# Kernel optimization log

Hardware: AMD Instinct MI355X
Metric: run time of the kernel (lower is better)

Reference implementation:

```python
import jax, jax.numpy as jnp
import numpy as np

B, S, H, F, E, K = 2, 2048, 1024, 2816, 8, 2

def setup_inputs() -> dict:
    key = jax.random.key(0)
    k0, k1, k2, k3, k4 = jax.random.split(key, 5)
    return {
        "hidden_states": jax.random.normal(k0, (B, S, H), dtype=jnp.float32),
        "router_w": jax.random.normal(k1, (E, H), dtype=jnp.float32) * (1.0 / np.sqrt(H)),
        "w_gate": jax.random.normal(k2, (E, H, F), dtype=jnp.float32) * (1.0 / np.sqrt(H)),
        "w_up": jax.random.normal(k3, (E, H, F), dtype=jnp.float32) * (1.0 / np.sqrt(H)),
        "w_down": jax.random.normal(k4, (E, F, H), dtype=jnp.float32) * (1.0 / np.sqrt(F)),
    }

def reference(hidden_states, router_w, w_gate, w_up, w_down):
    # Router: logits [B,S,E], top-k routing with softmax over the k selected logits.
    router_logits = jnp.einsum("bsh,eh->bse", hidden_states, router_w)
    topk_values, topk_indices = jax.lax.top_k(router_logits, K)  # [B,S,K]
    topk_weights = jax.nn.softmax(topk_values.astype(jnp.float32), axis=-1).astype(hidden_states.dtype)

    x = hidden_states.reshape(-1, H)            # [T,H], T = B*S
    flat_idx = topk_indices.reshape(-1, K)      # [T,K] (int)
    flat_w = topk_weights.reshape(-1, K)        # [T,K]

    mixed = jnp.zeros_like(x)
    for e in range(E):  # small fixed expert loop; tokens fully vectorized
        # per-token combine weight for expert e (0 if not routed here)
        w_e = jnp.sum(jnp.where(flat_idx == e, flat_w, jnp.zeros_like(flat_w)), axis=-1)[:, None]
        # SwiGLU expert MLP: down(silu(gate(x)) * up(x))
        y = (jax.nn.silu(x @ w_gate[e]) * (x @ w_up[e])) @ w_down[e]
        mixed = mixed + w_e * y
    mixed_output = mixed.reshape(hidden_states.shape)

    # Load-balancing aux loss (Switch-style)
    router_probs = jax.nn.softmax(router_logits.astype(jnp.float32), axis=-1)
    P = router_probs.mean(axis=(0, 1))                                   # [E]
    f = jax.nn.one_hot(topk_indices, E, dtype=jnp.float32).mean(axis=(0, 1, 2))  # [E]
    aux_loss = E * jnp.sum(f * P)
    return mixed_output, aux_loss
```

## Files before the change

### kernel.cpp

```cpp
#include <hip/hip_runtime.h>
#include <hip/hip_bf16.h>
#include <stdint.h>

#define T_TOK 4096
#define H_DIM 1024
#define F_DIM 2816
#define E_NUM 8
#define ROWS_CAP 9216
#define TOTAL_MT 72

typedef float  f32x4  __attribute__((ext_vector_type(4)));
typedef __bf16 bf16x8 __attribute__((ext_vector_type(8)));

__device__ __forceinline__ unsigned short f32_bf16(float f) {
  union { float f; unsigned u; } v; v.f = f;
  unsigned r = v.u + 0x7fffu + ((v.u >> 16) & 1u);
  return (unsigned short)(r >> 16);
}

__device__ __forceinline__ void async16(const void* g, void* l) {
  __builtin_amdgcn_global_load_lds(
      (__attribute__((address_space(1))) void*)(g),
      (__attribute__((address_space(3))) void*)(l),
      16, 0, 0);
}

__device__ __forceinline__ f32x4 mfma16(bf16x8 a, bf16x8 b, f32x4 c) {
  return __builtin_amdgcn_mfma_f32_16x16x32_bf16(a, b, c, 0, 0, 0);
}


__global__ __launch_bounds__(256) void conv_x_kernel(const float* __restrict__ x,
                                                     unsigned short* __restrict__ xb) {
  int i = blockIdx.x * 256 + threadIdx.x;
  float4 v = ((const float4*)x)[i];
  ushort4 o;
  o.x = f32_bf16(v.x); o.y = f32_bf16(v.y); o.z = f32_bf16(v.z); o.w = f32_bf16(v.w);
  ((ushort4*)xb)[i] = o;
}

__global__ __launch_bounds__(256) void transpose_conv(const float* __restrict__ src,
                                                      unsigned short* __restrict__ dst,
                                                      int R, int C) {
  __shared__ float tile[32][33];
  int e = blockIdx.z;
  const float* s = src + (size_t)e * R * C;
  unsigned short* d = dst + (size_t)e * R * C;
  int r0 = blockIdx.y * 32, c0 = blockIdx.x * 32;
  int tx = threadIdx.x, ty = threadIdx.y;
#pragma unroll
  for (int k = 0; k < 4; k++)
    tile[ty + 8 * k][tx] = s[(size_t)(r0 + ty + 8 * k) * C + (c0 + tx)];
  __syncthreads();
#pragma unroll
  for (int k = 0; k < 4; k++)
    d[(size_t)(c0 + ty + 8 * k) * R + (r0 + tx)] = f32_bf16(tile[tx][ty + 8 * k]);
}


__global__ __launch_bounds__(256) void router_kernel(const float* __restrict__ x,
                                                     const float* __restrict__ rw,
                                                     int* __restrict__ t2i,
                                                     float* __restrict__ t2w,
                                                     int* __restrict__ counts,
                                                     float* __restrict__ psum) {
  __shared__ float srw[E_NUM * H_DIM];
  __shared__ float sP[E_NUM];
  __shared__ int sC[E_NUM];
  int tid = threadIdx.x;
  for (int i = tid; i < E_NUM * H_DIM; i += 256) srw[i] = rw[i];
  if (tid < E_NUM) { sP[tid] = 0.f; sC[tid] = 0; }
  __syncthreads();
  int w = tid >> 6, lane = tid & 63;
  for (int it = 0; it < 16; ++it) {
    int t = blockIdx.x * 64 + w * 16 + it;
    float acc[E_NUM];
#pragma unroll
    for (int e = 0; e < E_NUM; e++) acc[e] = 0.f;
    const float* xr = x + (size_t)t * H_DIM;
    for (int h = lane; h < H_DIM; h += 64) {
      float xv = xr[h];
#pragma unroll
      for (int e = 0; e < E_NUM; e++) acc[e] += xv * srw[e * H_DIM + h];
    }
#pragma unroll
    for (int e = 0; e < E_NUM; e++) {
      float v = acc[e];
      for (int o = 32; o > 0; o >>= 1) v += __shfl_down(v, o, 64);
      acc[e] = __shfl(v, 0, 64);
    }
    if (lane == 0) {
      float mx = acc[0];
#pragma unroll
      for (int e = 1; e < E_NUM; e++) mx = fmaxf(mx, acc[e]);
      float pr[E_NUM], s = 0.f;
#pragma unroll
      for (int e = 0; e < E_NUM; e++) { pr[e] = __expf(acc[e] - mx); s += pr[e]; }
      float inv = 1.f / s;
#pragma unroll
      for (int e = 0; e < E_NUM; e++) atomicAdd(&sP[e], pr[e] * inv);
      int i0 = 0; float v0 = acc[0];
#pragma unroll
      for (int e = 1; e < E_NUM; e++) if (acc[e] > v0) { v0 = acc[e]; i0 = e; }
      int i1 = -1; float v1 = -3.4e38f;
#pragma unroll
      for (int e = 0; e < E_NUM; e++) if (e != i0 && acc[e] > v1) { v1 = acc[e]; i1 = e; }
      float e1 = __expf(v1 - v0);
      float w0 = 1.f / (1.f + e1);
      t2i[2 * t] = i0; t2i[2 * t + 1] = i1;
      t2w[2 * t] = w0; t2w[2 * t + 1] = e1 * w0;
      atomicAdd(&sC[i0], 1); atomicAdd(&sC[i1], 1);
    }
  }
  __syncthreads();
  if (tid < E_NUM) { atomicAdd(&counts[tid], sC[tid]); atomicAdd(&psum[tid], sP[tid]); }
}

__global__ void scan_aux_kernel(const int* __restrict__ counts, const float* __restrict__ psum,
                                int* __restrict__ offsets, int* __restrict__ cursors,
                                float* __restrict__ aux_out) {
  if (threadIdx.x == 0 && blockIdx.x == 0) {
    int off = 0; float aux = 0.f;
    for (int e = 0; e < E_NUM; e++) {
      offsets[e] = off;
      cursors[e] = off;
      off += (counts[e] + 127) & ~127;
      aux += ((float)counts[e] / 8192.0f) * (psum[e] / 4096.0f);
    }
    offsets[E_NUM] = off;
    *aux_out = 8.0f * aux;
  }
}

__global__ __launch_bounds__(256) void assign_kernel(const int* __restrict__ t2i,
                                                     const float* __restrict__ t2w,
                                                     int* __restrict__ cursors,
                                                     int* __restrict__ row2token,
                                                     float* __restrict__ roww) {
  int t = blockIdx.x * 256 + threadIdx.x;
#pragma unroll
  for (int s = 0; s < 2; s++) {
    int e = t2i[2 * t + s];
    int p = atomicAdd(&cursors[e], 1);
    row2token[p] = t;
    roww[p] = t2w[2 * t + s];
  }
}

__device__ __forceinline__ int find_expert(const int* __restrict__ offsets, int row0,
                                           int& off_out) {
  int esel = -1, off = 0;
#pragma unroll
  for (int e = 0; e < E_NUM; e++) {
    int lo = offsets[e], hi = offsets[e + 1];
    if (row0 >= lo && row0 < hi) { esel = e; off = lo; }
  }
  off_out = off;
  return esel;
}

__global__ __launch_bounds__(256) void gateup_kernel(
    const unsigned short* __restrict__ xb,
    const unsigned short* __restrict__ wgt,
    const unsigned short* __restrict__ wut,
    unsigned short* __restrict__ act,
    const int* __restrict__ counts, const int* __restrict__ offsets,
    const int* __restrict__ row2token) {
  int g = blockIdx.x;
  int row0 = g * 128;
  int off;
  int e = find_expert(offsets, row0, off);
  if (e < 0) return;
  int cnt = counts[e];
  int rowbase = row0 - off;
  int ntile = blockIdx.y;

  __shared__ __align__(16) unsigned short smA[128 * 32];
  __shared__ __align__(16) unsigned short smG[64 * 32];
  __shared__ __align__(16) unsigned short smU[64 * 32];

  int tid = threadIdx.x;
  int w = tid >> 6, lane = tid & 63;
  int wm = w & 1, wn = w >> 1;

  int cA0 = w * 64 + lane;
  int rA0 = cA0 >> 2, qA0 = cA0 & 3;
  int rA1 = rA0 + 64;
  int tok0 = (rowbase + rA0 < cnt) ? row2token[off + rowbase + rA0] : 0;
  int tok1 = (rowbase + rA1 < cnt) ? row2token[off + rowbase + rA1] : 0;
  const unsigned short* gA0 = xb + (size_t)tok0 * H_DIM + qA0 * 8;
  const unsigned short* gA1 = xb + (size_t)tok1 * H_DIM + qA0 * 8;
  size_t wb = (size_t)e * F_DIM * H_DIM;
  int rB = cA0 >> 2, qB = cA0 & 3;
  const unsigned short* gG = wgt + wb + (size_t)(ntile * 64 + rB) * H_DIM + qB * 8;
  const unsigned short* gU = wut + wb + (size_t)(ntile * 64 + rB) * H_DIM + qB * 8;
  unsigned short* lA0 = smA + (w * 64) * 8;
  unsigned short* lA1 = smA + (256 + w * 64) * 8;
  unsigned short* lG = smG + (w * 64) * 8;
  unsigned short* lU = smU + (w * 64) * 8;

  f32x4 accg[4][2], accu[4][2];
#pragma unroll
  for (int i = 0; i < 4; i++)
#pragma unroll
    for (int j = 0; j < 2; j++) {
      accg[i][j] = (f32x4){0.f, 0.f, 0.f, 0.f};
      accu[i][j] = (f32x4){0.f, 0.f, 0.f, 0.f};
    }

  int m = lane & 15, quad = lane >> 4;
  for (int k0 = 0; k0 < H_DIM; k0 += 32) {
    async16(gA0 + k0, lA0);
    async16(gA1 + k0, lA1);
    async16(gG + k0, lG);
    async16(gU + k0, lU);
    __syncthreads();
    bf16x8 a[4], bg[2], bu[2];
#pragma unroll
    for (int i = 0; i < 4; i++)
      a[i] = *(const bf16x8*)(smA + (wm * 64 + 16 * i + m) * 32 + quad * 8);
#pragma unroll
    for (int j = 0; j < 2; j++) {
      bg[j] = *(const bf16x8*)(smG + (wn * 32 + 16 * j + m) * 32 + quad * 8);
      bu[j] = *(const bf16x8*)(smU + (wn * 32 + 16 * j + m) * 32 + quad * 8);
    }
#pragma unroll
    for (int i = 0; i < 4; i++)
#pragma unroll
      for (int j = 0; j < 2; j++) {
        accg[i][j] = mfma16(a[i], bg[j], accg[i][j]);
        accu[i][j] = mfma16(a[i], bu[j], accu[i][j]);
      }
    __syncthreads();
  }

#pragma unroll
  for (int i = 0; i < 4; i++)
#pragma unroll
    for (int j = 0; j < 2; j++)
#pragma unroll
      for (int r = 0; r < 4; r++) {
        int rt = wm * 64 + 16 * i + quad * 4 + r;
        int ct = wn * 32 + 16 * j + m;
        float g2 = accg[i][j][r], u = accu[i][j][r];
        float sv = g2 / (1.f + __expf(-g2)) * u;
        act[(size_t)(off + rowbase + rt) * F_DIM + ntile * 64 + ct] = f32_bf16(sv);
      }
}

__global__ __launch_bounds__(256) void down_kernel(
    const unsigned short* __restrict__ act,
    const unsigned short* __restrict__ wdt,
    const int* __restrict__ counts, const int* __restrict__ offsets,
    const int* __restrict__ row2token, const float* __restrict__ roww,
    float* __restrict__ out) {
  int g = blockIdx.x;
  int row0 = g * 128;
  int off;
  int e = find_expert(offsets, row0, off);
  if (e < 0) return;
  int cnt = counts[e];
  int rowbase = row0 - off;
  int ntile = blockIdx.y;

  __shared__ __align__(16) unsigned short smA[128 * 32];
  __shared__ __align__(16) unsigned short smB[128 * 32];

  int tid = threadIdx.x;
  int w = tid >> 6, lane = tid & 63;
  int wm = w & 1, wn = w >> 1;

  int c0 = w * 64 + lane;
  int r0 = c0 >> 2, q0 = c0 & 3;
  int r1 = r0 + 64;
  const unsigned short* gA0 = act + (size_t)(off + rowbase + r0) * F_DIM + q0 * 8;
  const unsigned short* gA1 = act + (size_t)(off + rowbase + r1) * F_DIM + q0 * 8;
  size_t wb = (size_t)e * H_DIM * F_DIM;
  const unsigned short* gB0 = wdt + wb + (size_t)(ntile * 128 + r0) * F_DIM + q0 * 8;
  const unsigned short* gB1 = wdt + wb + (size_t)(ntile * 128 + r1) * F_DIM + q0 * 8;
  unsigned short* lA0 = smA + (w * 64) * 8;
  unsigned short* lA1 = smA + (256 + w * 64) * 8;
  unsigned short* lB0 = smB + (w * 64) * 8;
  unsigned short* lB1 = smB + (256 + w * 64) * 8;

  f32x4 acc[4][4];
#pragma unroll
  for (int i = 0; i < 4; i++)
#pragma unroll
    for (int j = 0; j < 4; j++) acc[i][j] = (f32x4){0.f, 0.f, 0.f, 0.f};

  int m = lane & 15, quad = lane >> 4;
  for (int k0 = 0; k0 < F_DIM; k0 += 32) {
    async16(gA0 + k0, lA0);
    async16(gA1 + k0, lA1);
    async16(gB0 + k0, lB0);
    async16(gB1 + k0, lB1);
    __syncthreads();
    bf16x8 a[4], b[4];
#pragma unroll
    for (int i = 0; i < 4; i++) {
      a[i] = *(const bf16x8*)(smA + (wm * 64 + 16 * i + m) * 32 + quad * 8);
      b[i] = *(const bf16x8*)(smB + (wn * 64 + 16 * i + m) * 32 + quad * 8);
    }
#pragma unroll
    for (int i = 0; i < 4; i++)
#pragma unroll
      for (int j = 0; j < 4; j++) acc[i][j] = mfma16(a[i], b[j], acc[i][j]);
    __syncthreads();
  }

#pragma unroll
  for (int i = 0; i < 4; i++)
#pragma unroll
    for (int r = 0; r < 4; r++) {
      int rt = wm * 64 + 16 * i + quad * 4 + r;
      int lrow = rowbase + rt;
      if (lrow < cnt) {
        int t = row2token[off + lrow];
        float cw = roww[off + lrow];
#pragma unroll
        for (int j = 0; j < 4; j++) {
          int h = ntile * 128 + wn * 64 + 16 * j + m;
          atomicAdd(out + (size_t)t * H_DIM + h, cw * acc[i][j][r]);
        }
      }
    }
}


extern "C" void kernel_launch(void* const* d_in, const int* in_sizes, int n_in,
                              void* d_out, int out_size, void* d_ws, size_t ws_size,
                              hipStream_t stream) {
  const float* x  = (const float*)d_in[0];
  const float* rw = (const float*)d_in[1];
  const float* wg = (const float*)d_in[2];
  const float* wu = (const float*)d_in[3];
  const float* wd = (const float*)d_in[4];
  float* out = (float*)d_out;

  char* ws = (char*)d_ws;
  size_t p = 0;
  auto alloc = [&](size_t bytes) {
    char* r = ws + p;
    p = (p + bytes + 255) & ~(size_t)255;
    return r;
  };
  unsigned short* Xb  = (unsigned short*)alloc((size_t)T_TOK * H_DIM * 2);
  unsigned short* Wgt = (unsigned short*)alloc((size_t)E_NUM * F_DIM * H_DIM * 2);
  unsigned short* Wut = (unsigned short*)alloc((size_t)E_NUM * F_DIM * H_DIM * 2);
  unsigned short* Wdt = (unsigned short*)alloc((size_t)E_NUM * H_DIM * F_DIM * 2);
  unsigned short* Act = (unsigned short*)alloc((size_t)ROWS_CAP * F_DIM * 2);
  int*   t2i = (int*)alloc(T_TOK * 2 * 4);
  float* t2w = (float*)alloc(T_TOK * 2 * 4);
  int*   row2token = (int*)alloc(ROWS_CAP * 4);
  float* roww = (float*)alloc(ROWS_CAP * 4);
  int* ctrs = (int*)alloc(64 * 4);
  int* counts  = ctrs;
  int* cursors = ctrs + 8;
  float* psum  = (float*)(ctrs + 16);
  int* offsets = ctrs + 24;

  hipMemsetAsync(out, 0, (size_t)T_TOK * H_DIM * 4, stream);
  hipMemsetAsync(ctrs, 0, 96, stream);

  conv_x_kernel<<<T_TOK * H_DIM / 4 / 256, 256, 0, stream>>>(x, Xb);
  transpose_conv<<<dim3(F_DIM / 32, H_DIM / 32, E_NUM), dim3(32, 8), 0, stream>>>(wg, Wgt, H_DIM, F_DIM);
  transpose_conv<<<dim3(F_DIM / 32, H_DIM / 32, E_NUM), dim3(32, 8), 0, stream>>>(wu, Wut, H_DIM, F_DIM);
  transpose_conv<<<dim3(H_DIM / 32, F_DIM / 32, E_NUM), dim3(32, 8), 0, stream>>>(wd, Wdt, F_DIM, H_DIM);

  router_kernel<<<T_TOK / 64, 256, 0, stream>>>(x, rw, t2i, t2w, counts, psum);
  scan_aux_kernel<<<1, 64, 0, stream>>>(counts, psum, offsets, cursors, out + (size_t)T_TOK * H_DIM);
  assign_kernel<<<T_TOK / 256, 256, 0, stream>>>(t2i, t2w, cursors, row2token, roww);

  gateup_kernel<<<dim3(TOTAL_MT, F_DIM / 64), 256, 0, stream>>>(Xb, Wgt, Wut, Act, counts, offsets, row2token);
  down_kernel<<<dim3(TOTAL_MT, H_DIM / 128), 256, 0, stream>>>(Act, Wdt, counts, offsets, row2token, roww, out);
}
```

Before: 721.3 us.

## Merge weight transposes, widen gate/up tile, replace atomics with combine pass

Fuses the three weight transpose-and-convert launches into one kernel that uses 64x64 tiles with float4 loads and ushort4 stores. Widens the gate/up GEMM N tile from 64 to 128 so each block reuses its A tile across more columns. Spreads the router over four times as many blocks. Replaces the float atomicAdd scatter in the down projection with per-row stores into a scratch buffer (aliased onto the dead Wgt region), followed by a combine kernel that sums each token's two rows. This removes the output memset and atomic contention, at the cost of an extra pass and more accumulator registers in gate/up.

```diff
diff --git a/kernel.cpp b/kernel.cpp
--- a/kernel.cpp
+++ b/kernel.cpp
@@ -39,22 +39,45 @@
   ((ushort4*)xb)[i] = o;
 }
 
-__global__ __launch_bounds__(256) void transpose_conv(const float* __restrict__ src,
-                                                      unsigned short* __restrict__ dst,
-                                                      int R, int C) {
-  __shared__ float tile[32][33];
-  int e = blockIdx.z;
-  const float* s = src + (size_t)e * R * C;
-  unsigned short* d = dst + (size_t)e * R * C;
-  int r0 = blockIdx.y * 32, c0 = blockIdx.x * 32;
-  int tx = threadIdx.x, ty = threadIdx.y;
-#pragma unroll
-  for (int k = 0; k < 4; k++)
-    tile[ty + 8 * k][tx] = s[(size_t)(r0 + ty + 8 * k) * C + (c0 + tx)];
+__global__ __launch_bounds__(256) void transpose_all(const float* __restrict__ wg,
+                                                     const float* __restrict__ wu,
+                                                     const float* __restrict__ wd,
+                                                     unsigned short* __restrict__ Wgt,
+                                                     unsigned short* __restrict__ Wut,
+                                                     unsigned short* __restrict__ Wdt) {
+  int mz = blockIdx.z >> 3, e = blockIdx.z & 7;
+  const float* s; unsigned short* d; int R, C;
+  size_t mat = (size_t)H_DIM * F_DIM;
+  if (mz == 0)      { s = wg + e * mat; d = Wgt + e * mat; R = H_DIM; C = F_DIM; }
+  else if (mz == 1) { s = wu + e * mat; d = Wut + e * mat; R = H_DIM; C = F_DIM; }
+  else              { s = wd + e * mat; d = Wdt + e * mat; R = F_DIM; C = H_DIM; }
+  int c0 = blockIdx.x * 64, r0 = blockIdx.y * 64;
+  if (c0 >= C || r0 >= R) return;
+
+  __shared__ float tile[64 * 65];
+  int tid = threadIdx.x;
+  int rr = tid >> 4, c4 = tid & 15;
+#pragma unroll
+  for (int it = 0; it < 4; it++) {
+    int r = rr + 16 * it;
+    float4 v = *(const float4*)(s + (size_t)(r0 + r) * C + c0 + c4 * 4);
+    tile[r * 65 + c4 * 4 + 0] = v.x;
+    tile[r * 65 + c4 * 4 + 1] = v.y;
+    tile[r * 65 + c4 * 4 + 2] = v.z;
+    tile[r * 65 + c4 * 4 + 3] = v.w;
+  }
   __syncthreads();
-#pragma unroll
-  for (int k = 0; k < 4; k++)
-    d[(size_t)(c0 + ty + 8 * k) * R + (r0 + tx)] = f32_bf16(tile[tx][ty + 8 * k]);
+  int cc = tid >> 4, r4 = tid & 15;
+#pragma unroll
+  for (int it = 0; it < 4; it++) {
+    int c = cc + 16 * it;
+    ushort4 o;
+    o.x = f32_bf16(tile[(r4 * 4 + 0) * 65 + c]);
+    o.y = f32_bf16(tile[(r4 * 4 + 1) * 65 + c]);
+    o.z = f32_bf16(tile[(r4 * 4 + 2) * 65 + c]);
+    o.w = f32_bf16(tile[(r4 * 4 + 3) * 65 + c]);
+    *(ushort4*)(d + (size_t)(c0 + c) * R + r0 + r4 * 4) = o;
+  }
 }
 
 
@@ -72,8 +95,8 @@
   if (tid < E_NUM) { sP[tid] = 0.f; sC[tid] = 0; }
   __syncthreads();
   int w = tid >> 6, lane = tid & 63;
-  for (int it = 0; it < 16; ++it) {
-    int t = blockIdx.x * 64 + w * 16 + it;
+  for (int it = 0; it < 4; ++it) {
+    int t = blockIdx.x * 16 + w * 4 + it;
     float acc[E_NUM];
 #pragma unroll
     for (int e = 0; e < E_NUM; e++) acc[e] = 0.f;
@@ -136,7 +159,8 @@
                                                      const float* __restrict__ t2w,
                                                      int* __restrict__ cursors,
                                                      int* __restrict__ row2token,
-                                                     float* __restrict__ roww) {
+                                                     float* __restrict__ roww,
+                                                     int* __restrict__ t2row) {
   int t = blockIdx.x * 256 + threadIdx.x;
 #pragma unroll
   for (int s = 0; s < 2; s++) {
@@ -144,6 +168,7 @@
     int p = atomicAdd(&cursors[e], 1);
     row2token[p] = t;
     roww[p] = t2w[2 * t + s];
+    t2row[2 * t + s] = p;
   }
 }
 
@@ -176,34 +201,36 @@
   int ntile = blockIdx.y;
 
   __shared__ __align__(16) unsigned short smA[128 * 32];
-  __shared__ __align__(16) unsigned short smG[64 * 32];
-  __shared__ __align__(16) unsigned short smU[64 * 32];
+  __shared__ __align__(16) unsigned short smG[128 * 32];
+  __shared__ __align__(16) unsigned short smU[128 * 32];
 
   int tid = threadIdx.x;
   int w = tid >> 6, lane = tid & 63;
   int wm = w & 1, wn = w >> 1;
 
-  int cA0 = w * 64 + lane;
-  int rA0 = cA0 >> 2, qA0 = cA0 & 3;
-  int rA1 = rA0 + 64;
-  int tok0 = (rowbase + rA0 < cnt) ? row2token[off + rowbase + rA0] : 0;
-  int tok1 = (rowbase + rA1 < cnt) ? row2token[off + rowbase + rA1] : 0;
-  const unsigned short* gA0 = xb + (size_t)tok0 * H_DIM + qA0 * 8;
-  const unsigned short* gA1 = xb + (size_t)tok1 * H_DIM + qA0 * 8;
+  int r0 = tid >> 2, q0 = tid & 3;
+  int r1 = r0 + 64;
+  int tok0 = (rowbase + r0 < cnt) ? row2token[off + rowbase + r0] : 0;
+  int tok1 = (rowbase + r1 < cnt) ? row2token[off + rowbase + r1] : 0;
+  const unsigned short* gA0 = xb + (size_t)tok0 * H_DIM + q0 * 8;
+  const unsigned short* gA1 = xb + (size_t)tok1 * H_DIM + q0 * 8;
   size_t wb = (size_t)e * F_DIM * H_DIM;
-  int rB = cA0 >> 2, qB = cA0 & 3;
-  const unsigned short* gG = wgt + wb + (size_t)(ntile * 64 + rB) * H_DIM + qB * 8;
-  const unsigned short* gU = wut + wb + (size_t)(ntile * 64 + rB) * H_DIM + qB * 8;
-  unsigned short* lA0 = smA + (w * 64) * 8;
-  unsigned short* lA1 = smA + (256 + w * 64) * 8;
-  unsigned short* lG = smG + (w * 64) * 8;
-  unsigned short* lU = smU + (w * 64) * 8;
-
-  f32x4 accg[4][2], accu[4][2];
+  const unsigned short* gG0 = wgt + wb + (size_t)(ntile * 128 + r0) * H_DIM + q0 * 8;
+  const unsigned short* gG1 = wgt + wb + (size_t)(ntile * 128 + r1) * H_DIM + q0 * 8;
+  const unsigned short* gU0 = wut + wb + (size_t)(ntile * 128 + r0) * H_DIM + q0 * 8;
+  const unsigned short* gU1 = wut + wb + (size_t)(ntile * 128 + r1) * H_DIM + q0 * 8;
+  unsigned short* lA0 = smA + tid * 8;
+  unsigned short* lA1 = smA + (tid + 256) * 8;
+  unsigned short* lG0 = smG + tid * 8;
+  unsigned short* lG1 = smG + (tid + 256) * 8;
+  unsigned short* lU0 = smU + tid * 8;
+  unsigned short* lU1 = smU + (tid + 256) * 8;
+
+  f32x4 accg[4][4], accu[4][4];
 #pragma unroll
   for (int i = 0; i < 4; i++)
 #pragma unroll
-    for (int j = 0; j < 2; j++) {
+    for (int j = 0; j < 4; j++) {
       accg[i][j] = (f32x4){0.f, 0.f, 0.f, 0.f};
       accu[i][j] = (f32x4){0.f, 0.f, 0.f, 0.f};
     }
@@ -212,22 +239,24 @@
   for (int k0 = 0; k0 < H_DIM; k0 += 32) {
     async16(gA0 + k0, lA0);
     async16(gA1 + k0, lA1);
-    async16(gG + k0, lG);
-    async16(gU + k0, lU);
+    async16(gG0 + k0, lG0);
+    async16(gG1 + k0, lG1);
+    async16(gU0 + k0, lU0);
+    async16(gU1 + k0, lU1);
     __syncthreads();
-    bf16x8 a[4], bg[2], bu[2];
+    bf16x8 a[4], bg[4], bu[4];
 #pragma unroll
     for (int i = 0; i < 4; i++)
       a[i] = *(const bf16x8*)(smA + (wm * 64 + 16 * i + m) * 32 + quad * 8);
 #pragma unroll
-    for (int j = 0; j < 2; j++) {
-      bg[j] = *(const bf16x8*)(smG + (wn * 32 + 16 * j + m) * 32 + quad * 8);
-      bu[j] = *(const bf16x8*)(smU + (wn * 32 + 16 * j + m) * 32 + quad * 8);
+    for (int j = 0; j < 4; j++) {
+      bg[j] = *(const bf16x8*)(smG + (wn * 64 + 16 * j + m) * 32 + quad * 8);
+      bu[j] = *(const bf16x8*)(smU + (wn * 64 + 16 * j + m) * 32 + quad * 8);
     }
 #pragma unroll
     for (int i = 0; i < 4; i++)
 #pragma unroll
-      for (int j = 0; j < 2; j++) {
+      for (int j = 0; j < 4; j++) {
         accg[i][j] = mfma16(a[i], bg[j], accg[i][j]);
         accu[i][j] = mfma16(a[i], bu[j], accu[i][j]);
       }
@@ -237,14 +266,14 @@
 #pragma unroll
   for (int i = 0; i < 4; i++)
 #pragma unroll
-    for (int j = 0; j < 2; j++)
+    for (int j = 0; j < 4; j++)
 #pragma unroll
       for (int r = 0; r < 4; r++) {
         int rt = wm * 64 + 16 * i + quad * 4 + r;
-        int ct = wn * 32 + 16 * j + m;
+        int ct = wn * 64 + 16 * j + m;
         float g2 = accg[i][j][r], u = accu[i][j][r];
         float sv = g2 / (1.f + __expf(-g2)) * u;
-        act[(size_t)(off + rowbase + rt) * F_DIM + ntile * 64 + ct] = f32_bf16(sv);
+        act[(size_t)(off + rowbase + rt) * F_DIM + ntile * 128 + ct] = f32_bf16(sv);
       }
 }
 
@@ -252,8 +281,8 @@
     const unsigned short* __restrict__ act,
     const unsigned short* __restrict__ wdt,
     const int* __restrict__ counts, const int* __restrict__ offsets,
-    const int* __restrict__ row2token, const float* __restrict__ roww,
-    float* __restrict__ out) {
+    const float* __restrict__ roww,
+    float* __restrict__ Y) {
   int g = blockIdx.x;
   int row0 = g * 128;
   int off;
@@ -270,18 +299,17 @@
   int w = tid >> 6, lane = tid & 63;
   int wm = w & 1, wn = w >> 1;
 
-  int c0 = w * 64 + lane;
-  int r0 = c0 >> 2, q0 = c0 & 3;
+  int r0 = tid >> 2, q0 = tid & 3;
   int r1 = r0 + 64;
   const unsigned short* gA0 = act + (size_t)(off + rowbase + r0) * F_DIM + q0 * 8;
   const unsigned short* gA1 = act + (size_t)(off + rowbase + r1) * F_DIM + q0 * 8;
   size_t wb = (size_t)e * H_DIM * F_DIM;
   const unsigned short* gB0 = wdt + wb + (size_t)(ntile * 128 + r0) * F_DIM + q0 * 8;
   const unsigned short* gB1 = wdt + wb + (size_t)(ntile * 128 + r1) * F_DIM + q0 * 8;
-  unsigned short* lA0 = smA + (w * 64) * 8;
-  unsigned short* lA1 = smA + (256 + w * 64) * 8;
-  unsigned short* lB0 = smB + (w * 64) * 8;
-  unsigned short* lB1 = smB + (256 + w * 64) * 8;
+  unsigned short* lA0 = smA + tid * 8;
+  unsigned short* lA1 = smA + (tid + 256) * 8;
+  unsigned short* lB0 = smB + tid * 8;
+  unsigned short* lB1 = smB + (tid + 256) * 8;
 
   f32x4 acc[4][4];
 #pragma unroll
@@ -316,15 +344,25 @@
       int rt = wm * 64 + 16 * i + quad * 4 + r;
       int lrow = rowbase + rt;
       if (lrow < cnt) {
-        int t = row2token[off + lrow];
         float cw = roww[off + lrow];
 #pragma unroll
         for (int j = 0; j < 4; j++) {
           int h = ntile * 128 + wn * 64 + 16 * j + m;
-          atomicAdd(out + (size_t)t * H_DIM + h, cw * acc[i][j][r]);
+          Y[(size_t)(off + lrow) * H_DIM + h] = cw * acc[i][j][r];
         }
       }
     }
+}
+
+__global__ __launch_bounds__(256) void combine_kernel(const float* __restrict__ Y,
+                                                      const int* __restrict__ t2row,
+                                                      float* __restrict__ out) {
+  int t = blockIdx.x, hc = threadIdx.x;
+  int r0 = t2row[2 * t], r1 = t2row[2 * t + 1];
+  float4 a = ((const float4*)(Y + (size_t)r0 * H_DIM))[hc];
+  float4 b = ((const float4*)(Y + (size_t)r1 * H_DIM))[hc];
+  float4 o; o.x = a.x + b.x; o.y = a.y + b.y; o.z = a.z + b.z; o.w = a.w + b.w;
+  ((float4*)(out + (size_t)t * H_DIM))[hc] = o;
 }
 
 
@@ -352,6 +390,7 @@
   unsigned short* Act = (unsigned short*)alloc((size_t)ROWS_CAP * F_DIM * 2);
   int*   t2i = (int*)alloc(T_TOK * 2 * 4);
   float* t2w = (float*)alloc(T_TOK * 2 * 4);
+  int*   t2row = (int*)alloc(T_TOK * 2 * 4);
   int*   row2token = (int*)alloc(ROWS_CAP * 4);
   float* roww = (float*)alloc(ROWS_CAP * 4);
   int* ctrs = (int*)alloc(64 * 4);
@@ -359,19 +398,18 @@
   int* cursors = ctrs + 8;
   float* psum  = (float*)(ctrs + 16);
   int* offsets = ctrs + 24;
-
-  hipMemsetAsync(out, 0, (size_t)T_TOK * H_DIM * 4, stream);
+  float* Y = (float*)Wgt;
+
   hipMemsetAsync(ctrs, 0, 96, stream);
 
   conv_x_kernel<<<T_TOK * H_DIM / 4 / 256, 256, 0, stream>>>(x, Xb);
-  transpose_conv<<<dim3(F_DIM / 32, H_DIM / 32, E_NUM), dim3(32, 8), 0, stream>>>(wg, Wgt, H_DIM, F_DIM);
-  transpose_conv<<<dim3(F_DIM / 32, H_DIM / 32, E_NUM), dim3(32, 8), 0, stream>>>(wu, Wut, H_DIM, F_DIM);
-  transpose_conv<<<dim3(H_DIM / 32, F_DIM / 32, E_NUM), dim3(32, 8), 0, stream>>>(wd, Wdt, F_DIM, H_DIM);
-
-  router_kernel<<<T_TOK / 64, 256, 0, stream>>>(x, rw, t2i, t2w, counts, psum);
+  transpose_all<<<dim3(F_DIM / 64, F_DIM / 64, 24), 256, 0, stream>>>(wg, wu, wd, Wgt, Wut, Wdt);
+
+  router_kernel<<<T_TOK / 16, 256, 0, stream>>>(x, rw, t2i, t2w, counts, psum);
   scan_aux_kernel<<<1, 64, 0, stream>>>(counts, psum, offsets, cursors, out + (size_t)T_TOK * H_DIM);
-  assign_kernel<<<T_TOK / 256, 256, 0, stream>>>(t2i, t2w, cursors, row2token, roww);
-
-  gateup_kernel<<<dim3(TOTAL_MT, F_DIM / 64), 256, 0, stream>>>(Xb, Wgt, Wut, Act, counts, offsets, row2token);
-  down_kernel<<<dim3(TOTAL_MT, H_DIM / 128), 256, 0, stream>>>(Act, Wdt, counts, offsets, row2token, roww, out);
-}
+  assign_kernel<<<T_TOK / 256, 256, 0, stream>>>(t2i, t2w, cursors, row2token, roww, t2row);
+
+  gateup_kernel<<<dim3(TOTAL_MT, F_DIM / 128), 256, 0, stream>>>(Xb, Wgt, Wut, Act, counts, offsets, row2token);
+  down_kernel<<<dim3(TOTAL_MT, H_DIM / 128), 256, 0, stream>>>(Act, Wdt, counts, offsets, roww, Y);
+  combine_kernel<<<T_TOK, 256, 0, stream>>>(Y, t2row, out);
+}
```

Result: no change. 708.1 us (-1.8%).
